# Performance work log

Measured on AMD Instinct MI355X. Metric: run time of the kernel, lower is better.

## Reference

```python
import jax, jax.numpy as jnp
import numpy as np

DIM = 768
HEADS = 12
HIDDEN = 4 * DIM
EPS = 1e-5


def _layernorm(x, g, b):
    mu = jnp.mean(x, axis=-1, keepdims=True)
    var = jnp.var(x, axis=-1, keepdims=True)
    return (x - mu) * jax.lax.rsqrt(var + EPS) * g + b


def setup_inputs() -> dict:
    key = jax.random.key(0)
    ks = jax.random.split(key, 8)
    B, N, C = 16, 577, DIM
    s = lambda fan: 1.0 / np.sqrt(fan)
    return {
        "x": jax.random.normal(ks[0], (B, N, C), jnp.float32),
        "ln1_g": jnp.ones((C,), jnp.float32),
        "ln1_b": jnp.zeros((C,), jnp.float32),
        "qkv_w": jax.random.normal(ks[1], (C, 3 * C), jnp.float32) * s(C),
        "qkv_b": jnp.zeros((3 * C,), jnp.float32),
        "proj_w": jax.random.normal(ks[2], (C, C), jnp.float32) * s(C),
        "proj_b": jnp.zeros((C,), jnp.float32),
        "ln2_g": jnp.ones((C,), jnp.float32),
        "ln2_b": jnp.zeros((C,), jnp.float32),
        "fc1_w": jax.random.normal(ks[3], (C, HIDDEN), jnp.float32) * s(C),
        "fc1_b": jnp.zeros((HIDDEN,), jnp.float32),
        "fc2_w": jax.random.normal(ks[4], (HIDDEN, C), jnp.float32) * s(HIDDEN),
        "fc2_b": jnp.zeros((C,), jnp.float32),
    }


def reference(x, ln1_g, ln1_b, qkv_w, qkv_b, proj_w, proj_b,
              ln2_g, ln2_b, fc1_w, fc1_b, fc2_w, fc2_b):
    B, N, C = x.shape
    H = HEADS
    Dh = C // H
    scale = Dh ** (-0.5)

    # --- attention branch (pre-norm) ---
    xn = _layernorm(x, ln1_g, ln1_b)
    qkv = xn @ qkv_w + qkv_b                         # [B,N,3C]
    qkv = qkv.reshape(B, N, 3, H, Dh).transpose(2, 0, 3, 1, 4)  # [3,B,H,N,Dh]
    q, k, v = qkv[0], qkv[1], qkv[2]
    attn = jax.nn.softmax(jnp.einsum('bhnd,bhmd->bhnm', q, k) * scale, axis=-1)
    y = jnp.einsum('bhnm,bhmd->bhnd', attn, v)       # [B,H,N,Dh]
    y = y.transpose(0, 2, 1, 3).reshape(B, N, C)
    y = y @ proj_w + proj_b
    x = x + y

    # --- MLP branch (pre-norm, exact GELU as torch default) ---
    xn2 = _layernorm(x, ln2_g, ln2_b)
    h = jax.nn.gelu(xn2 @ fc1_w + fc1_b, approximate=False)
    x = x + (h @ fc2_w + fc2_b)
    return x
```

## Files before the change

kernel.cpp:

```cpp
#include <hip/hip_runtime.h>
#include <hip/hip_bf16.h>
#include <math.h>


#define C_DIM   768
#define SEQ     577
#define BATCH   16
#define NHEAD   12
#define DHEAD   64
#define MREAL   (BATCH*SEQ)
#define MPAD    9472
#define HID     3072
#define QKW     1536
#define NKV     640
#define QSCALE  0.1803368801111204f

typedef __hip_bfloat16 bf16;
typedef __attribute__((ext_vector_type(8))) short v8s;
typedef __attribute__((ext_vector_type(4))) float v4f;

static __device__ __forceinline__ bf16 f2b(float f){ return __float2bfloat16(f); }
static __device__ __forceinline__ float us2f(unsigned short u){
  union{ float f; unsigned int i; } x; x.i = ((unsigned int)u)<<16; return x.f;
}
static __device__ __forceinline__ short f2s(float f){
  bf16 t = __float2bfloat16(f); return *(short*)&t;
}
static __device__ __forceinline__ float gelu_fast(float x){
  float z2 = 2.302585092994046f * x * (1.f + 0.044715f*x*x);
  return x / (1.f + exp2f(-z2));
}


__global__ __launch_bounds__(256) void k_transpose_cast(
    const float* __restrict__ src, bf16* __restrict__ dst, int R, int C)
{
  __shared__ float s[64][65];
  const int tr = blockIdx.x*64, tc = blockIdx.y*64;
  const int t = threadIdx.x;
  const int lr = t >> 4, lc4 = t & 15;
  #pragma unroll
  for (int i=0;i<4;i++){
    int r = lr + i*16;
    float4 v = *(const float4*)(src + (size_t)(tr+r)*C + tc + lc4*4);
    s[r][lc4*4+0]=v.x; s[r][lc4*4+1]=v.y; s[r][lc4*4+2]=v.z; s[r][lc4*4+3]=v.w;
  }
  __syncthreads();
  const int c = t >> 2, seg = t & 3;
  alignas(16) bf16 tmp[16];
  #pragma unroll
  for (int j=0;j<16;j++) tmp[j] = f2b(s[seg*16+j][c]);
  bf16* dp = dst + (size_t)(tc+c)*R + tr + seg*16;
  *(uint4*)dp       = *(uint4*)tmp;
  *(uint4*)(dp + 8) = *(uint4*)(tmp + 8);
}

__global__ __launch_bounds__(256) void k_layernorm(
    const float* __restrict__ in, const float* __restrict__ g,
    const float* __restrict__ b, bf16* __restrict__ o)
{
  int row = blockIdx.x, tid = threadIdx.x;
  size_t base = (size_t)row*C_DIM;
  if (row >= MREAL){
    #pragma unroll
    for (int j=0;j<3;j++) o[base + tid + j*256] = f2b(0.f);
    return;
  }
  float v[3], s=0.f, ss=0.f;
  #pragma unroll
  for (int j=0;j<3;j++){ v[j] = in[base + tid + j*256]; s += v[j]; ss += v[j]*v[j]; }
  #pragma unroll
  for (int off=32; off>0; off>>=1){ s += __shfl_xor(s,off); ss += __shfl_xor(ss,off); }
  __shared__ float red[8];
  int wv = tid>>6;
  if ((tid&63)==0){ red[wv] = s; red[4+wv] = ss; }
  __syncthreads();
  float S  = red[0]+red[1]+red[2]+red[3];
  float SS = red[4]+red[5]+red[6]+red[7];
  float mu   = S*(1.f/C_DIM);
  float rstd = rsqrtf(SS*(1.f/C_DIM) - mu*mu + 1e-5f);
  #pragma unroll
  for (int j=0;j<3;j++){
    int c = tid + j*256;
    o[base+c] = f2b((v[j]-mu)*rstd*g[c] + b[c]);
  }
}

__global__ __launch_bounds__(256) void k_reduce2_ln(
    const bf16* __restrict__ P, const float* __restrict__ bias,
    const float* __restrict__ resid, float* __restrict__ out,
    const float* __restrict__ g, const float* __restrict__ bln,
    bf16* __restrict__ xn2)
{
  int row = blockIdx.x, tid = threadIdx.x;
  size_t base = (size_t)row*C_DIM;
  if (row >= MREAL){
    #pragma unroll
    for (int j=0;j<3;j++) xn2[base + tid + j*256] = f2b(0.f);
    return;
  }
  const unsigned short* P0 = (const unsigned short*)P;
  const unsigned short* P1 = P0 + (size_t)MPAD*C_DIM;
  float v[3], s=0.f, ss=0.f;
  #pragma unroll
  for (int j=0;j<3;j++){
    int c = tid + j*256;
    size_t idx = base + c;
    float val = us2f(P0[idx]) + us2f(P1[idx]) + bias[c] + resid[idx];
    out[idx] = val; v[j] = val; s += val; ss += val*val;
  }
  #pragma unroll
  for (int off=32; off>0; off>>=1){ s += __shfl_xor(s,off); ss += __shfl_xor(ss,off); }
  __shared__ float red[8];
  int wv = tid>>6;
  if ((tid&63)==0){ red[wv] = s; red[4+wv] = ss; }
  __syncthreads();
  float S  = red[0]+red[1]+red[2]+red[3];
  float SS = red[4]+red[5]+red[6]+red[7];
  float mu   = S*(1.f/C_DIM);
  float rstd = rsqrtf(SS*(1.f/C_DIM) - mu*mu + 1e-5f);
  #pragma unroll
  for (int j=0;j<3;j++){
    int c = tid + j*256;
    xn2[base+c] = f2b((v[j]-mu)*rstd*g[c] + bln[c]);
  }
}

__global__ __launch_bounds__(256) void k_reduce2(
    const bf16* __restrict__ P, const float* __restrict__ bias,
    const float* __restrict__ resid, float* __restrict__ out)
{
  size_t i = ((size_t)blockIdx.x*256 + threadIdx.x)*8;
  int c = (int)(i % C_DIM);
  v8s p0 = *(const v8s*)(P + i);
  v8s p1 = *(const v8s*)(P + (size_t)MPAD*C_DIM + i);
  float r[8];
  #pragma unroll
  for (int j=0;j<8;j++) r[j] = resid[i+j];
  #pragma unroll
  for (int j=0;j<8;j++)
    out[i+j] = us2f((unsigned short)p0[j]) + us2f((unsigned short)p1[j])
             + bias[c+j] + r[j];
}

__global__ __launch_bounds__(256, 3) void k_flash(
    const bf16* __restrict__ qk, const bf16* __restrict__ VtAll,
    bf16* __restrict__ y)
{
  __shared__ alignas(16) bf16 sK[2][64*64];
  __shared__ alignas(16) bf16 sV[2][64*64];
  __shared__ alignas(16) bf16 sP[4][16*72];

  const int tid = threadIdx.x;
  const int wave = tid>>6, lane = tid&63;
  const int r16 = lane&15, kg = lane>>4;

  const int id = blockIdx.x;
  const int swz = (id&7)*240 + (id>>3);
  const int hh = swz/10, qt = swz - hh*10;
  const int b_ = hh/NHEAD, h_ = hh - b_*NHEAD;

  const int qrow = b_*SEQ + qt*64 + wave*16 + r16;
  v8s qf[2];
  qf[0] = *(const v8s*)(qk + (size_t)qrow*QKW + h_*DHEAD + kg*8);
  qf[1] = *(const v8s*)(qk + (size_t)qrow*QKW + h_*DHEAD + 32 + kg*8);

  auto stage = [&](int kt, int buf){
    #pragma unroll
    for (int i=0;i<2;i++){
      int chunk = i*256 + tid;
      int row = chunk>>3, ch = chunk&7;
      int sc = ch ^ (row&7);
      const bf16* gk = qk + (size_t)(b_*SEQ + kt*64 + row)*QKW
                          + C_DIM + h_*DHEAD + sc*8;
      const bf16* gv = VtAll + (size_t)(b_*C_DIM + h_*DHEAD + row)*NKV
                             + kt*64 + sc*8;
      __builtin_amdgcn_global_load_lds(
          (const __attribute__((address_space(1))) void*)gk,
          (__attribute__((address_space(3))) void*)((char*)&sK[buf][0] + i*4096 + wave*1024),
          16, 0, 0);
      __builtin_amdgcn_global_load_lds(
          (const __attribute__((address_space(1))) void*)gv,
          (__attribute__((address_space(3))) void*)((char*)&sV[buf][0] + i*4096 + wave*1024),
          16, 0, 0);
    }
  };

  float m_run = -1e30f, l_run = 0.f;
  v4f zero4 = {0.f,0.f,0.f,0.f};
  v4f o[4] = {zero4, zero4, zero4, zero4};

  stage(0, 0);
  for (int kt=0; kt<10; ++kt){
    __syncthreads();
    if (kt < 9) stage(kt+1, (kt+1)&1);
    const bf16* Kt = &sK[kt&1][0];
    const bf16* Vt = &sV[kt&1][0];

    v4f sfr[4] = {zero4, zero4, zero4, zero4};
    #pragma unroll
    for (int ks=0; ks<2; ++ks){
      #pragma unroll
      for (int m=0;m<4;m++){
        int key = m*16 + r16;
        v8s kf = *(const v8s*)(Kt + key*64 + (((ks*4+kg) ^ (key&7))*8));
        sfr[m] = __builtin_amdgcn_mfma_f32_16x16x32_bf16(kf, qf[ks], sfr[m], 0, 0, 0);
      }
    }

    if (kt == 9){
      #pragma unroll
      for (int m=0;m<4;m++)
        #pragma unroll
        for (int gg=0; gg<4; ++gg){
          int kb = 576 + m*16 + kg*4 + gg;
          if (kb >= SEQ) sfr[m][gg] = -1e30f;
        }
    }

    float tmax = -1e30f;
    #pragma unroll
    for (int m=0;m<4;m++)
      #pragma unroll
      for (int gg=0; gg<4; ++gg) tmax = fmaxf(tmax, sfr[m][gg]);
    tmax = fmaxf(tmax, __shfl_xor(tmax, 16));
    tmax = fmaxf(tmax, __shfl_xor(tmax, 32));
    float mn  = fmaxf(m_run, tmax);
    float scl = exp2f(m_run - mn);
    float ps  = 0.f;
    #pragma unroll
    for (int m=0;m<4;m++)
      #pragma unroll
      for (int gg=0; gg<4; ++gg){
        float pv = exp2f(sfr[m][gg] - mn);
        sfr[m][gg] = pv; ps += pv;
      }
    ps += __shfl_xor(ps, 16);
    ps += __shfl_xor(ps, 32);
    l_run = l_run*scl + ps;
    m_run = mn;
    #pragma unroll
    for (int mf=0; mf<4; ++mf) o[mf] *= scl;

    bf16* Pw = &sP[wave][0];
    #pragma unroll
    for (int m=0;m<4;m++){
      short4 w;
      w.x = f2s(sfr[m][0]); w.y = f2s(sfr[m][1]);
      w.z = f2s(sfr[m][2]); w.w = f2s(sfr[m][3]);
      *(short4*)(Pw + r16*72 + m*16 + kg*4) = w;
    }
    asm volatile("s_waitcnt lgkmcnt(0)" ::: "memory");
    v8s pb0 = *(const v8s*)(Pw + r16*72 + kg*8);
    v8s pb1 = *(const v8s*)(Pw + r16*72 + 32 + kg*8);
    #pragma unroll
    for (int mf=0; mf<4; ++mf){
      int d = mf*16 + r16;
      v8s v0 = *(const v8s*)(Vt + d*64 + ((kg     ^ (d&7))*8));
      v8s v1 = *(const v8s*)(Vt + d*64 + (((4+kg) ^ (d&7))*8));
      o[mf] = __builtin_amdgcn_mfma_f32_16x16x32_bf16(v0, pb0, o[mf], 0, 0, 0);
      o[mf] = __builtin_amdgcn_mfma_f32_16x16x32_bf16(v1, pb1, o[mf], 0, 0, 0);
    }
  }

  const int qg = qt*64 + wave*16 + r16;
  if (qg < SEQ){
    float inv = 1.f / l_run;
    #pragma unroll
    for (int mf=0; mf<4; ++mf){
      short4 w;
      w.x = f2s(o[mf][0]*inv); w.y = f2s(o[mf][1]*inv);
      w.z = f2s(o[mf][2]*inv); w.w = f2s(o[mf][3]*inv);
      *(short4*)(y + (size_t)(b_*SEQ + qg)*C_DIM + h_*DHEAD + mf*16 + kg*4) = w;
    }
  }
}

template<int EPI>
__global__ __launch_bounds__(256, 4) void gemm_bt(
    const bf16* __restrict__ A, int lda,
    const bf16* __restrict__ BT, int ldb,
    void* Cv, int ldc,
    const float* __restrict__ bias,
    const float* resid,
    int K)
{
  __shared__ alignas(16) bf16 sA[128*64];
  __shared__ alignas(16) bf16 sB[128*64];
  const int tid  = threadIdx.x;
  const int wave = tid>>6, lane = tid&63;
  const int wr = wave>>1, wc = wave&1;
  const int r16 = lane&15, kg = lane>>4;

  int nx = gridDim.x, nwg = nx*gridDim.y;
  int id = blockIdx.y*nx + blockIdx.x;
  int qq = nwg>>3, r8 = nwg&7, xcd = id&7, j = id>>3;
  int swz = (xcd<r8 ? xcd*(qq+1) : r8*(qq+1) + (xcd-r8)*qq) + j;
  int mt = swz / nx, nt = swz % nx;

  int kb = 0;
  if constexpr (EPI==6) kb = blockIdx.z * K;

  v4f acc[4][4];
  v4f zero4 = {0.f,0.f,0.f,0.f};
  #pragma unroll
  for (int m=0;m<4;m++)
    #pragma unroll
    for (int n=0;n<4;n++) acc[m][n] = zero4;

  const int mrow0 = mt*128, ncol0 = nt*128;

  for (int kt=0; kt<K; kt+=64){
    #pragma unroll
    for (int i=0;i<4;i++){
      int ci = wave*4 + i;
      int q  = ci*64 + lane;
      int rr = q>>3;
      int cc = (q&7)*8;
      const bf16* ga = A  + (size_t)(mrow0+rr)*lda + (kb+kt+cc);
      const bf16* gb = BT + (size_t)(ncol0+rr)*ldb + (kb+kt+cc);
      __builtin_amdgcn_global_load_lds(
          (const __attribute__((address_space(1))) void*)ga,
          (__attribute__((address_space(3))) void*)((char*)sA + ci*1024), 16, 0, 0);
      __builtin_amdgcn_global_load_lds(
          (const __attribute__((address_space(1))) void*)gb,
          (__attribute__((address_space(3))) void*)((char*)sB + ci*1024), 16, 0, 0);
    }
    __syncthreads();
    #pragma unroll
    for (int ks=0; ks<2; ks++){
      v8s av[4], bv[4];
      #pragma unroll
      for (int m=0;m<4;m++)
        av[m] = *(const v8s*)(sA + (wr*64 + m*16 + r16)*64 + ks*32 + kg*8);
      #pragma unroll
      for (int n=0;n<4;n++)
        bv[n] = *(const v8s*)(sB + (wc*64 + n*16 + r16)*64 + ks*32 + kg*8);
      #pragma unroll
      for (int m=0;m<4;m++)
        #pragma unroll
        for (int n=0;n<4;n++)
          acc[m][n] = __builtin_amdgcn_mfma_f32_16x16x32_bf16(av[m], bv[n], acc[m][n], 0, 0, 0);
    }
    __syncthreads();
  }

  #pragma unroll
  for (int m=0;m<4;m++){
    #pragma unroll
    for (int n=0;n<4;n++){
      int col = ncol0 + wc*64 + n*16 + r16;
      #pragma unroll
      for (int gg=0; gg<4; gg++){
        int row = mrow0 + wr*64 + m*16 + kg*4 + gg;
        float v = acc[m][n][gg];
        if constexpr (EPI==0){
          float oo = v + bias[col];
          if (col < C_DIM) oo *= QSCALE;
          ((bf16*)Cv)[(size_t)row*ldc + col] = f2b(oo);
        } else if constexpr (EPI==1){
          ((bf16*)Cv)[(size_t)row*ldc + col] = f2b(gelu_fast(v + bias[col]));
        } else if constexpr (EPI==5){
          int g = col;
          if (g < MREAL){
            int b = g / SEQ;
            int key = g - b*SEQ;
            ((bf16*)Cv)[((size_t)b*C_DIM + row)*NKV + key] = f2b(v + bias[row]);
          }
        } else {
          ((bf16*)Cv)[(size_t)blockIdx.z*MPAD*C_DIM + (size_t)row*ldc + col] = f2b(v);
        }
      }
    }
  }
}


extern "C" void kernel_launch(void* const* d_in, const int* in_sizes, int n_in,
                              void* d_out, int out_size, void* d_ws, size_t ws_size,
                              hipStream_t stream)
{
  const float* x     = (const float*)d_in[0];
  const float* ln1g  = (const float*)d_in[1];
  const float* ln1b  = (const float*)d_in[2];
  const float* qkvw  = (const float*)d_in[3];
  const float* qkvb  = (const float*)d_in[4];
  const float* projw = (const float*)d_in[5];
  const float* projb = (const float*)d_in[6];
  const float* ln2g  = (const float*)d_in[7];
  const float* ln2b  = (const float*)d_in[8];
  const float* fc1w  = (const float*)d_in[9];
  const float* fc1b  = (const float*)d_in[10];
  const float* fc2w  = (const float*)d_in[11];
  const float* fc2b  = (const float*)d_in[12];
  float* out = (float*)d_out;

  char* p = (char*)d_ws;
  auto take = [&](size_t n){ char* r = p; p += (n + 255) & ~(size_t)255; return r; };
  bf16* qkvT = (bf16*)take((size_t)(3*C_DIM)*C_DIM*2);
  bf16* projT= (bf16*)take((size_t)C_DIM*C_DIM*2);
  bf16* fc1T = (bf16*)take((size_t)HID*C_DIM*2);
  bf16* fc2T = (bf16*)take((size_t)C_DIM*HID*2);
  bf16* xn   = (bf16*)take((size_t)MPAD*C_DIM*2);
  bf16* xn2  = (bf16*)take((size_t)MPAD*C_DIM*2);
  bf16* qk   = (bf16*)take((size_t)MPAD*QKW*2);
  bf16* y    = (bf16*)take((size_t)MPAD*C_DIM*2);
  bf16* h    = (bf16*)take((size_t)MPAD*HID*2);
  bf16* VtAll= (bf16*)take((size_t)(BATCH*C_DIM + 2*DHEAD)*NKV*2);
  bf16* P    = qk;

  k_transpose_cast<<<dim3(C_DIM/64, 3*C_DIM/64), 256, 0, stream>>>(qkvw, qkvT, C_DIM, 3*C_DIM);
  k_transpose_cast<<<dim3(C_DIM/64, C_DIM/64),  256, 0, stream>>>(projw, projT, C_DIM, C_DIM);
  k_transpose_cast<<<dim3(C_DIM/64, HID/64),    256, 0, stream>>>(fc1w, fc1T, C_DIM, HID);
  k_transpose_cast<<<dim3(HID/64,  C_DIM/64),   256, 0, stream>>>(fc2w, fc2T, HID, C_DIM);

  k_layernorm<<<MPAD, 256, 0, stream>>>(x, ln1g, ln1b, xn);

  gemm_bt<0><<<dim3(QKW/128, MPAD/128), 256, 0, stream>>>(
      xn, C_DIM, qkvT, C_DIM, qk, QKW, qkvb, nullptr, C_DIM);

  gemm_bt<5><<<dim3(MPAD/128, C_DIM/128), 256, 0, stream>>>(
      qkvT + (size_t)QKW*C_DIM, C_DIM, xn, C_DIM, VtAll, 0,
      qkvb + 2*C_DIM, nullptr, C_DIM);

  k_flash<<<1920, 256, 0, stream>>>(qk, VtAll, y);

  gemm_bt<6><<<dim3(C_DIM/128, MPAD/128, 2), 256, 0, stream>>>(
      y, C_DIM, projT, C_DIM, P, C_DIM, nullptr, nullptr, C_DIM/2);
  k_reduce2_ln<<<MPAD, 256, 0, stream>>>(P, projb, x, out, ln2g, ln2b, xn2);

  gemm_bt<1><<<dim3(HID/128, MPAD/128), 256, 0, stream>>>(
      xn2, C_DIM, fc1T, C_DIM, h, HID, fc1b, nullptr, C_DIM);

  gemm_bt<6><<<dim3(C_DIM/128, MPAD/128, 2), 256, 0, stream>>>(
      h, HID, fc2T, HID, P, C_DIM, nullptr, nullptr, HID/2);
  k_reduce2<<<(MREAL*C_DIM)/(256*8), 256, 0, stream>>>(P, fc2b, out, out);
}
```

Before: 300.8 us.

## Use 32x32 MFMA GEMM with XCD swizzle for fc1 and merge weight transposes

Adds a dedicated fc1 GEMM kernel built on 32x32x16 bf16 MFMA instructions. It uses direct global-to-LDS loads and an XCD-aware block swizzle, and applies the GELU epilogue in place of the 16x16 generic GEMM. It also merges the four weight transpose/cast launches into one kernel to cut launch overhead. The new GEMM has no LDS double buffering and could hit LDS bank conflicts from its unpadded layout.

```diff
diff --git a/kernel.cpp b/kernel.cpp
--- a/kernel.cpp
+++ b/kernel.cpp
@@ -18,6 +18,7 @@
 typedef __hip_bfloat16 bf16;
 typedef __attribute__((ext_vector_type(8))) short v8s;
 typedef __attribute__((ext_vector_type(4))) float v4f;
+typedef __attribute__((ext_vector_type(16))) float v16f;
 
 static __device__ __forceinline__ bf16 f2b(float f){ return __float2bfloat16(f); }
 static __device__ __forceinline__ float us2f(unsigned short u){
@@ -31,12 +32,21 @@
   return x / (1.f + exp2f(-z2));
 }
 
-
-__global__ __launch_bounds__(256) void k_transpose_cast(
-    const float* __restrict__ src, bf16* __restrict__ dst, int R, int C)
-{
+__global__ __launch_bounds__(256) void k_transpose_all(
+    const float* __restrict__ qkvw, const float* __restrict__ projw,
+    const float* __restrict__ fc1w, const float* __restrict__ fc2w,
+    bf16* __restrict__ qkvT, bf16* __restrict__ projT,
+    bf16* __restrict__ fc1T, bf16* __restrict__ fc2T)
+{
+  int id = blockIdx.x;
+  const float* src; bf16* dst; int R, C, nx;
+  if (id < 432)      { src=qkvw; dst=qkvT; R=768;  C=2304; nx=36; }
+  else if (id < 576) { id-=432; src=projw; dst=projT; R=768;  C=768;  nx=12; }
+  else if (id < 1152){ id-=576; src=fc1w;  dst=fc1T;  R=768;  C=3072; nx=48; }
+  else               { id-=1152; src=fc2w; dst=fc2T;  R=3072; C=768;  nx=12; }
+  const int tr = (id/nx)*64, tc = (id%nx)*64;
+
   __shared__ float s[64][65];
-  const int tr = blockIdx.x*64, tc = blockIdx.y*64;
   const int t = threadIdx.x;
   const int lr = t >> 4, lc4 = t & 15;
   #pragma unroll
@@ -358,8 +368,6 @@
           float oo = v + bias[col];
           if (col < C_DIM) oo *= QSCALE;
           ((bf16*)Cv)[(size_t)row*ldc + col] = f2b(oo);
-        } else if constexpr (EPI==1){
-          ((bf16*)Cv)[(size_t)row*ldc + col] = f2b(gelu_fast(v + bias[col]));
         } else if constexpr (EPI==5){
           int g = col;
           if (g < MREAL){
@@ -370,6 +378,85 @@
         } else {
           ((bf16*)Cv)[(size_t)blockIdx.z*MPAD*C_DIM + (size_t)row*ldc + col] = f2b(v);
         }
+      }
+    }
+  }
+}
+
+__global__ __launch_bounds__(256, 4) void gemm_bt32(
+    const bf16* __restrict__ A, int lda,
+    const bf16* __restrict__ BT, int ldb,
+    bf16* __restrict__ Cv, int ldc,
+    const float* __restrict__ bias,
+    int K)
+{
+  __shared__ alignas(16) bf16 sA[128*64];
+  __shared__ alignas(16) bf16 sB[128*64];
+  const int tid  = threadIdx.x;
+  const int wave = tid>>6, lane = tid&63;
+  const int wr = wave>>1, wc = wave&1;
+  const int l31 = lane&31, lh = lane>>5;
+
+  int nx = gridDim.x, nwg = nx*gridDim.y;
+  int id = blockIdx.y*nx + blockIdx.x;
+  int qq = nwg>>3, r8 = nwg&7, xcd = id&7, j = id>>3;
+  int swz = (xcd<r8 ? xcd*(qq+1) : r8*(qq+1) + (xcd-r8)*qq) + j;
+  int mt = swz / nx, nt = swz % nx;
+  const int mrow0 = mt*128, ncol0 = nt*128;
+
+  v16f acc[2][2];
+  #pragma unroll
+  for (int i=0;i<2;i++)
+    #pragma unroll
+    for (int jn=0;jn<2;jn++)
+      #pragma unroll
+      for (int r=0;r<16;r++) acc[i][jn][r] = 0.f;
+
+  for (int kt=0; kt<K; kt+=64){
+    #pragma unroll
+    for (int i=0;i<4;i++){
+      int ci = wave*4 + i;
+      int q  = ci*64 + lane;
+      int rr = q>>3;
+      int cc = (q&7)*8;
+      const bf16* ga = A  + (size_t)(mrow0+rr)*lda + (kt+cc);
+      const bf16* gb = BT + (size_t)(ncol0+rr)*ldb + (kt+cc);
+      __builtin_amdgcn_global_load_lds(
+          (const __attribute__((address_space(1))) void*)ga,
+          (__attribute__((address_space(3))) void*)((char*)sA + ci*1024), 16, 0, 0);
+      __builtin_amdgcn_global_load_lds(
+          (const __attribute__((address_space(1))) void*)gb,
+          (__attribute__((address_space(3))) void*)((char*)sB + ci*1024), 16, 0, 0);
+    }
+    __syncthreads();
+    #pragma unroll
+    for (int ks=0; ks<4; ks++){
+      v8s a[2], b[2];
+      #pragma unroll
+      for (int i=0;i<2;i++)
+        a[i] = *(const v8s*)(sA + (wr*64 + i*32 + l31)*64 + ks*16 + lh*8);
+      #pragma unroll
+      for (int jn=0;jn<2;jn++)
+        b[jn] = *(const v8s*)(sB + (wc*64 + jn*32 + l31)*64 + ks*16 + lh*8);
+      #pragma unroll
+      for (int i=0;i<2;i++)
+        #pragma unroll
+        for (int jn=0;jn<2;jn++)
+          acc[i][jn] = __builtin_amdgcn_mfma_f32_32x32x16_bf16(a[i], b[jn], acc[i][jn], 0, 0, 0);
+    }
+    __syncthreads();
+  }
+
+  #pragma unroll
+  for (int i=0;i<2;i++){
+    #pragma unroll
+    for (int jn=0;jn<2;jn++){
+      int col = ncol0 + wc*64 + jn*32 + l31;
+      float bcol = bias[col];
+      #pragma unroll
+      for (int r=0;r<16;r++){
+        int row = mrow0 + wr*64 + i*32 + (r&3) + 8*(r>>2) + 4*lh;
+        Cv[(size_t)row*ldc + col] = f2b(gelu_fast(acc[i][jn][r] + bcol));
       }
     }
   }
@@ -409,10 +496,8 @@
   bf16* VtAll= (bf16*)take((size_t)(BATCH*C_DIM + 2*DHEAD)*NKV*2);
   bf16* P    = qk;
 
-  k_transpose_cast<<<dim3(C_DIM/64, 3*C_DIM/64), 256, 0, stream>>>(qkvw, qkvT, C_DIM, 3*C_DIM);
-  k_transpose_cast<<<dim3(C_DIM/64, C_DIM/64),  256, 0, stream>>>(projw, projT, C_DIM, C_DIM);
-  k_transpose_cast<<<dim3(C_DIM/64, HID/64),    256, 0, stream>>>(fc1w, fc1T, C_DIM, HID);
-  k_transpose_cast<<<dim3(HID/64,  C_DIM/64),   256, 0, stream>>>(fc2w, fc2T, HID, C_DIM);
+  k_transpose_all<<<1728, 256, 0, stream>>>(qkvw, projw, fc1w, fc2w,
+                                            qkvT, projT, fc1T, fc2T);
 
   k_layernorm<<<MPAD, 256, 0, stream>>>(x, ln1g, ln1b, xn);
 
@@ -429,8 +514,8 @@
       y, C_DIM, projT, C_DIM, P, C_DIM, nullptr, nullptr, C_DIM/2);
   k_reduce2_ln<<<MPAD, 256, 0, stream>>>(P, projb, x, out, ln2g, ln2b, xn2);
 
-  gemm_bt<1><<<dim3(HID/128, MPAD/128), 256, 0, stream>>>(
-      xn2, C_DIM, fc1T, C_DIM, h, HID, fc1b, nullptr, C_DIM);
+  gemm_bt32<<<dim3(HID/128, MPAD/128), 256, 0, stream>>>(
+      xn2, C_DIM, fc1T, C_DIM, h, HID, fc1b, C_DIM);
 
   gemm_bt<6><<<dim3(C_DIM/128, MPAD/128, 2), 256, 0, stream>>>(
       h, HID, fc2T, HID, P, C_DIM, nullptr, nullptr, HID/2);
```

Result: slower. 319.8 us (+6.3%).
